# Optimization experiments

Hardware: AMD Instinct MI355X
Metric: run time of the kernel (lower is better)

The kernel has to match this reference:

```python
import jax, jax.numpy as jnp
import numpy as np

VOCAB = 32000
D = 512        # input_dim == hid_dim
HID = 512
LAYERS = 2
B = 64
S = 2048
PAD = 0


def setup_inputs() -> dict:
    key = jax.random.key(0)
    ks = jax.random.split(key, 6)
    # indices in [1, VOCAB) so the padding row is never hit (PAD=0)
    src = jax.random.randint(ks[0], (B, S), 1, VOCAB, dtype=jnp.int64 if jax.config.read('jax_enable_x64') else jnp.int32)
    scale = 1.0 / np.sqrt(HID)
    embed = jax.random.normal(ks[1], (VOCAB, D), dtype=jnp.float32)
    embed = embed.at[PAD].set(0.0)  # padding_idx row is zero
    # nn.RNN weights: per layer W_ih [HID, in], W_hh [HID, HID], b_ih, b_hh [HID]
    W_ih = jax.random.uniform(ks[2], (LAYERS, HID, D), jnp.float32, -scale, scale)
    W_hh = jax.random.uniform(ks[3], (LAYERS, HID, HID), jnp.float32, -scale, scale)
    b_ih = jax.random.uniform(ks[4], (LAYERS, HID), jnp.float32, -scale, scale)
    b_hh = jax.random.uniform(ks[5], (LAYERS, HID), jnp.float32, -scale, scale)
    return {"src": src, "embed": embed, "W_ih": W_ih, "W_hh": W_hh,
            "b_ih": b_ih, "b_hh": b_hh}


def reference(src, embed, W_ih, W_hh, b_ih, b_hh):
    # src: [B, S] -> transpose to time-major [S, B], then embedding lookup
    x = embed[src.T]                      # [S, B, D]
    finals = []
    for l in range(LAYERS):
        wi, wh = W_ih[l], W_hh[l]
        bi, bh = b_ih[l], b_hh[l]
        xb = jnp.einsum('sbd,hd->sbh', x, wi) + bi + bh  # precompute input term
        def step(h, x_t):
            h_new = jnp.tanh(x_t + h @ wh.T)
            return h_new, h_new
        h0 = jnp.zeros((x.shape[1], HID), dtype=x.dtype)
        hT, ys = jax.lax.scan(step, h0, xb)
        finals.append(hT)
        x = ys                             # feed layer output to next layer
    # nn.RNN returns hidden of shape [n_layers, batch, hid_dim]
    return jnp.stack(finals, axis=0)
```

## Files before the change

kernel.cpp:

```cpp
#include <hip/hip_runtime.h>


#define SEQ 2048

typedef _Float16 half8 __attribute__((ext_vector_type(8)));
typedef float floatx4 __attribute__((ext_vector_type(4)));
typedef unsigned long long u64;

__device__ inline half8 cvt8(const float* p) {
    float4 f0 = ((const float4*)p)[0];
    float4 f1 = ((const float4*)p)[1];
    half8 h;
    h[0]=(_Float16)f0.x; h[1]=(_Float16)f0.y; h[2]=(_Float16)f0.z; h[3]=(_Float16)f0.w;
    h[4]=(_Float16)f1.x; h[5]=(_Float16)f1.y; h[6]=(_Float16)f1.z; h[7]=(_Float16)f1.w;
    return h;
}

__device__ inline u64 ld8(const void* p) {
    return __hip_atomic_load((const u64*)p, __ATOMIC_RELAXED, __HIP_MEMORY_SCOPE_AGENT);
}
__device__ inline half8 ldfrag(const _Float16* p) {
    union { u64 d[2]; half8 h; } u;
    u.d[0] = ld8(p);
    u.d[1] = ld8(p + 4);
    return u.h;
}

#define MFMA(a, b, c) __builtin_amdgcn_mfma_f32_16x16x32_f16((a), (b), (c), 0, 0, 0)

__global__ __launch_bounds__(256, 1)
void rnn_persist(const int* __restrict__ src, const float* __restrict__ embed,
                 const float* __restrict__ W_ih, const float* __restrict__ W_hh,
                 const float* __restrict__ b_ih, const float* __restrict__ b_hh,
                 float* __restrict__ out, _Float16* hbase, int* flags)
{
    const int tid = threadIdx.x;
    if (tid >= 64) return;

    const int lane = tid;
    const int g    = blockIdx.x;
    const int L    = g >> 7;
    const int bg   = (g >> 5) & 3;
    const int jg   = g & 31;
    const int q    = lane >> 4;
    const int rr   = lane & 15;
    const int col  = jg * 16 + rr;

    _Float16* h0s = hbase;
    _Float16* h1s = hbase + 4 * 64 * 512;

    half8 bw[32];
    {
        const float* Wi = W_ih + ((size_t)L * 512 + col) * 512;
        const float* Wh = W_hh + ((size_t)L * 512 + col) * 512;
        #pragma unroll
        for (int u = 0; u < 16; ++u) bw[u]      = cvt8(Wi + u * 32 + q * 8);
        #pragma unroll
        for (int u = 0; u < 16; ++u) bw[16 + u] = cvt8(Wh + u * 32 + q * 8);
    }
    const float bias = b_ih[L * 512 + col] + b_hh[L * 512 + col];

    const int arow = bg * 16 + rr;
    int* flg = flags + bg * 64;
    const int lf = lane >> 5;

    for (int t = 0; t < SEQ; ++t) {
        floatx4 acc0 = {0.f,0.f,0.f,0.f}, acc1 = {0.f,0.f,0.f,0.f};

        if (L == 0) {
            const int erow = src[arow * SEQ + t];
            const float* eb = embed + (size_t)erow * 512 + q * 8;
            half8 ax[16];
            #pragma unroll
            for (int u = 0; u < 16; ++u) ax[u] = cvt8(eb + u * 32);
            #pragma unroll
            for (int u = 0; u < 16; ++u) {
                if (u & 1) acc1 = MFMA(ax[u], bw[u], acc1);
                else       acc0 = MFMA(ax[u], bw[u], acc0);
            }
            const int tgt = (lf == 0) ? t : (t - 3);
            for (long it = 0; it < (1L << 26); ++it) {
                int v = __hip_atomic_load(&flg[lane], __ATOMIC_RELAXED,
                                          __HIP_MEMORY_SCOPE_AGENT);
                if (__ballot(v >= tgt) == ~0ull) break;
                __builtin_amdgcn_s_sleep(1);
            }
            __atomic_signal_fence(__ATOMIC_SEQ_CST);
            if (t > 0) {
                const _Float16* hb = h0s + ((t - 1) & 3) * (64 * 512)
                                   + arow * 512 + q * 8;
                half8 ah[16];
                #pragma unroll
                for (int u = 0; u < 16; ++u) ah[u] = ldfrag(hb + u * 32);
                #pragma unroll
                for (int u = 0; u < 16; ++u) {
                    if (u & 1) acc1 = MFMA(ah[u], bw[16 + u], acc1);
                    else       acc0 = MFMA(ah[u], bw[16 + u], acc0);
                }
            }
        } else {
            const int tgt = (lf == 0) ? (t + 1) : t;
            for (long it = 0; it < (1L << 26); ++it) {
                int v = __hip_atomic_load(&flg[lane], __ATOMIC_RELAXED,
                                          __HIP_MEMORY_SCOPE_AGENT);
                if (__ballot(v >= tgt) == ~0ull) break;
                __builtin_amdgcn_s_sleep(1);
            }
            __atomic_signal_fence(__ATOMIC_SEQ_CST);
            {
                const _Float16* xa = h0s + (t & 3) * (64 * 512)
                                   + arow * 512 + q * 8;
                half8 ax[16];
                #pragma unroll
                for (int u = 0; u < 16; ++u) ax[u] = ldfrag(xa + u * 32);
                #pragma unroll
                for (int u = 0; u < 16; ++u) {
                    if (u & 1) acc1 = MFMA(ax[u], bw[u], acc1);
                    else       acc0 = MFMA(ax[u], bw[u], acc0);
                }
            }
            if (t > 0) {
                const _Float16* hb = h1s + ((t - 1) & 3) * (64 * 512)
                                   + arow * 512 + q * 8;
                half8 ah[16];
                #pragma unroll
                for (int u = 0; u < 16; ++u) ah[u] = ldfrag(hb + u * 32);
                #pragma unroll
                for (int u = 0; u < 16; ++u) {
                    if (u & 1) acc1 = MFMA(ah[u], bw[16 + u], acc1);
                    else       acc0 = MFMA(ah[u], bw[16 + u], acc0);
                }
            }
        }

        float hv[4];
        #pragma unroll
        for (int r = 0; r < 4; ++r)
            hv[r] = tanhf(acc0[r] + acc1[r] + bias);

        if (t == SEQ - 1) {
            #pragma unroll
            for (int r = 0; r < 4; ++r)
                out[(size_t)L * 64 * 512 + (size_t)(bg * 16 + q * 4 + r) * 512 + col]
                    = hv[r];
        }

        {
            _Float16* hw = ((L == 0) ? h0s : h1s) + (t & 3) * (64 * 512)
                         + (size_t)(bg * 16) * 512 + col;
            #pragma unroll
            for (int r = 0; r < 4; ++r) {
                union { _Float16 f; unsigned short u; } cv;
                cv.f = (_Float16)hv[r];
                __hip_atomic_store((unsigned short*)(hw + (q * 4 + r) * 512),
                                   cv.u, __ATOMIC_RELAXED,
                                   __HIP_MEMORY_SCOPE_AGENT);
            }
        }
        __atomic_signal_fence(__ATOMIC_SEQ_CST);
        __builtin_amdgcn_s_waitcnt(0);
        __atomic_signal_fence(__ATOMIC_SEQ_CST);
        if (lane == 0)
            __hip_atomic_store(&flg[L * 32 + jg], t + 1, __ATOMIC_RELAXED,
                               __HIP_MEMORY_SCOPE_AGENT);
    }
}

extern "C" void kernel_launch(void* const* d_in, const int* in_sizes, int n_in,
                              void* d_out, int out_size, void* d_ws, size_t ws_size,
                              hipStream_t stream) {
    const int*   src   = (const int*)  d_in[0];
    const float* embed = (const float*)d_in[1];
    const float* W_ih  = (const float*)d_in[2];
    const float* W_hh  = (const float*)d_in[3];
    const float* b_ih  = (const float*)d_in[4];
    const float* b_hh  = (const float*)d_in[5];
    float*     out   = (float*)d_out;
    int*       flags = (int*)d_ws;
    _Float16*  hbase = (_Float16*)((char*)d_ws + 16384);

    hipMemsetAsync(d_ws, 0, 16384, stream);

    rnn_persist<<<dim3(256), dim3(256), 0, stream>>>(
        src, embed, W_ih, W_hh, b_ih, b_hh, out, hbase, flags);
}
```

Before: 15.58 ms.

## Place each batch group's RNN tiles on one XCD with plain volatile sync

Each block reads its XCD id, and a grid-wide barrier lets every block see the full block-to-XCD map. The four XCDs holding the most blocks each take one batch group, and four waves per block each run a tile, so all producer/consumer flag and hidden-state traffic for a batch group stays inside one XCD's L2. Within an XCD the flags and hidden states use plain volatile loads and stores instead of agent-scope atomics. The next step's embedding load is also moved after the flag store so it overlaps the wait. The change relies on same-XCD L2 coherence for volatile accesses and adds a startup barrier. If the map is unsuitable it falls back to the atomic path, and both paths gain a spin timeout that can silently abort.

```diff
diff --git a/kernel.cpp b/kernel.cpp
--- a/kernel.cpp
+++ b/kernel.cpp
@@ -6,6 +6,8 @@
 typedef _Float16 half8 __attribute__((ext_vector_type(8)));
 typedef float floatx4 __attribute__((ext_vector_type(4)));
 typedef unsigned long long u64;
+
+#define MFMA(a, b, c) __builtin_amdgcn_mfma_f32_16x16x32_f16((a), (b), (c), 0, 0, 0)
 
 __device__ inline half8 cvt8(const float* p) {
     float4 f0 = ((const float4*)p)[0];
@@ -16,38 +18,53 @@
     return h;
 }
 
-__device__ inline u64 ld8(const void* p) {
-    return __hip_atomic_load((const u64*)p, __ATOMIC_RELAXED, __HIP_MEMORY_SCOPE_AGENT);
-}
-__device__ inline half8 ldfrag(const _Float16* p) {
-    union { u64 d[2]; half8 h; } u;
-    u.d[0] = ld8(p);
-    u.d[1] = ld8(p + 4);
-    return u.h;
-}
-
-#define MFMA(a, b, c) __builtin_amdgcn_mfma_f32_16x16x32_f16((a), (b), (c), 0, 0, 0)
-
-__global__ __launch_bounds__(256, 1)
-void rnn_persist(const int* __restrict__ src, const float* __restrict__ embed,
-                 const float* __restrict__ W_ih, const float* __restrict__ W_hh,
-                 const float* __restrict__ b_ih, const float* __restrict__ b_hh,
-                 float* __restrict__ out, _Float16* hbase, int* flags)
+__device__ inline int xcc_id(void) {
+    int x;
+    asm volatile("s_getreg_b32 %0, hwreg(HW_REG_XCC_ID)" : "=s"(x));
+    return x & 7;
+}
+
+__device__ inline int f_ldflag(const int* p) { return *(volatile const int*)p; }
+__device__ inline void f_stflag(int* p, int v) { *(volatile int*)p = v; }
+__device__ inline void f_sth2(_Float16* p, _Float16 v) { *(volatile _Float16*)p = v; }
+__device__ inline void f_ldfrag(const _Float16* p, half8 a[16]) {
+    #pragma unroll
+    for (int u = 0; u < 16; ++u) a[u] = *(volatile const half8*)(p + u * 32);
+}
+
+__device__ inline int a_ldflag(const int* p) {
+    return __hip_atomic_load(p, __ATOMIC_RELAXED, __HIP_MEMORY_SCOPE_AGENT);
+}
+__device__ inline void a_stflag(int* p, int v) {
+    __hip_atomic_store(p, v, __ATOMIC_RELAXED, __HIP_MEMORY_SCOPE_AGENT);
+}
+__device__ inline void a_sth2(_Float16* p, _Float16 v) {
+    union { _Float16 f; unsigned short s; } c; c.f = v;
+    __hip_atomic_store((unsigned short*)p, c.s, __ATOMIC_RELAXED,
+                       __HIP_MEMORY_SCOPE_AGENT);
+}
+__device__ inline void a_ldfrag(const _Float16* p, half8 a[16]) {
+    #pragma unroll
+    for (int u = 0; u < 16; ++u) {
+        union { u64 d[2]; half8 h; } x;
+        x.d[0] = __hip_atomic_load((const u64*)(p + u * 32),
+                                   __ATOMIC_RELAXED, __HIP_MEMORY_SCOPE_AGENT);
+        x.d[1] = __hip_atomic_load((const u64*)(p + u * 32) + 1,
+                                   __ATOMIC_RELAXED, __HIP_MEMORY_SCOPE_AGENT);
+        a[u] = x.h;
+    }
+}
+
+template <bool FAST>
+__device__ void run_rnn(int L, int jg, int bg, int lane,
+                        const int* __restrict__ src, const float* __restrict__ embed,
+                        const float* __restrict__ W_ih, const float* __restrict__ W_hh,
+                        const float* __restrict__ b_ih, const float* __restrict__ b_hh,
+                        float* __restrict__ out, _Float16* hbase, int* flags)
 {
-    const int tid = threadIdx.x;
-    if (tid >= 64) return;
-
-    const int lane = tid;
-    const int g    = blockIdx.x;
-    const int L    = g >> 7;
-    const int bg   = (g >> 5) & 3;
-    const int jg   = g & 31;
-    const int q    = lane >> 4;
-    const int rr   = lane & 15;
-    const int col  = jg * 16 + rr;
-
-    _Float16* h0s = hbase;
-    _Float16* h1s = hbase + 4 * 64 * 512;
+    const int q   = lane >> 4;
+    const int rr  = lane & 15;
+    const int col = jg * 16 + rr;
 
     half8 bw[32];
     {
@@ -60,38 +77,42 @@
     }
     const float bias = b_ih[L * 512 + col] + b_hh[L * 512 + col];
 
-    const int arow = bg * 16 + rr;
-    int* flg = flags + bg * 64;
-    const int lf = lane >> 5;
-
-    for (int t = 0; t < SEQ; ++t) {
+    _Float16* hbg = hbase + (size_t)bg * 65536;
+    int* flg   = flags + bg * 1024;
+    int* stamp = flg + L * 32 + jg;
+
+    half8 ax[16];
+    if (L == 0) {
+        const int erow = src[(bg * 16 + rr) * SEQ + 0];
+        const float* eb = embed + (size_t)erow * 512 + q * 8;
+        #pragma unroll
+        for (int u = 0; u < 16; ++u) ax[u] = cvt8(eb + u * 32);
+    }
+
+    bool dead = false;
+    for (int t = 0; t < SEQ && !dead; ++t) {
         floatx4 acc0 = {0.f,0.f,0.f,0.f}, acc1 = {0.f,0.f,0.f,0.f};
 
         if (L == 0) {
-            const int erow = src[arow * SEQ + t];
-            const float* eb = embed + (size_t)erow * 512 + q * 8;
-            half8 ax[16];
-            #pragma unroll
-            for (int u = 0; u < 16; ++u) ax[u] = cvt8(eb + u * 32);
             #pragma unroll
             for (int u = 0; u < 16; ++u) {
                 if (u & 1) acc1 = MFMA(ax[u], bw[u], acc1);
                 else       acc0 = MFMA(ax[u], bw[u], acc0);
             }
-            const int tgt = (lf == 0) ? t : (t - 3);
-            for (long it = 0; it < (1L << 26); ++it) {
-                int v = __hip_atomic_load(&flg[lane], __ATOMIC_RELAXED,
-                                          __HIP_MEMORY_SCOPE_AGENT);
+            const int tgt = (lane < 32) ? t : (t - 3);
+            int it = 0;
+            while (true) {
+                int v = FAST ? f_ldflag(flg + lane) : a_ldflag(flg + lane);
                 if (__ballot(v >= tgt) == ~0ull) break;
+                if (++it > (1 << 22)) { dead = true; break; }
                 __builtin_amdgcn_s_sleep(1);
             }
+            if (dead) break;
             __atomic_signal_fence(__ATOMIC_SEQ_CST);
             if (t > 0) {
-                const _Float16* hb = h0s + ((t - 1) & 3) * (64 * 512)
-                                   + arow * 512 + q * 8;
+                const _Float16* hp = hbg + ((t - 1) & 3) * 8192 + rr * 512 + q * 8;
                 half8 ah[16];
-                #pragma unroll
-                for (int u = 0; u < 16; ++u) ah[u] = ldfrag(hb + u * 32);
+                if (FAST) f_ldfrag(hp, ah); else a_ldfrag(hp, ah);
                 #pragma unroll
                 for (int u = 0; u < 16; ++u) {
                     if (u & 1) acc1 = MFMA(ah[u], bw[16 + u], acc1);
@@ -99,32 +120,31 @@
                 }
             }
         } else {
-            const int tgt = (lf == 0) ? (t + 1) : t;
-            for (long it = 0; it < (1L << 26); ++it) {
-                int v = __hip_atomic_load(&flg[lane], __ATOMIC_RELAXED,
-                                          __HIP_MEMORY_SCOPE_AGENT);
+            const int tgt = (lane < 32) ? (t + 1) : t;
+            int it = 0;
+            while (true) {
+                int v = FAST ? f_ldflag(flg + lane) : a_ldflag(flg + lane);
                 if (__ballot(v >= tgt) == ~0ull) break;
+                if (++it > (1 << 22)) { dead = true; break; }
                 __builtin_amdgcn_s_sleep(1);
             }
+            if (dead) break;
             __atomic_signal_fence(__ATOMIC_SEQ_CST);
             {
-                const _Float16* xa = h0s + (t & 3) * (64 * 512)
-                                   + arow * 512 + q * 8;
-                half8 ax[16];
-                #pragma unroll
-                for (int u = 0; u < 16; ++u) ax[u] = ldfrag(xa + u * 32);
+                const _Float16* xp = hbg + (t & 3) * 8192 + rr * 512 + q * 8;
+                half8 xa[16];
+                if (FAST) f_ldfrag(xp, xa); else a_ldfrag(xp, xa);
                 #pragma unroll
                 for (int u = 0; u < 16; ++u) {
-                    if (u & 1) acc1 = MFMA(ax[u], bw[u], acc1);
-                    else       acc0 = MFMA(ax[u], bw[u], acc0);
+                    if (u & 1) acc1 = MFMA(xa[u], bw[u], acc1);
+                    else       acc0 = MFMA(xa[u], bw[u], acc0);
                 }
             }
             if (t > 0) {
-                const _Float16* hb = h1s + ((t - 1) & 3) * (64 * 512)
-                                   + arow * 512 + q * 8;
+                const _Float16* hp = hbg + 32768 + ((t - 1) & 3) * 8192
+                                   + rr * 512 + q * 8;
                 half8 ah[16];
-                #pragma unroll
-                for (int u = 0; u < 16; ++u) ah[u] = ldfrag(hb + u * 32);
+                if (FAST) f_ldfrag(hp, ah); else a_ldfrag(hp, ah);
                 #pragma unroll
                 for (int u = 0; u < 16; ++u) {
                     if (u & 1) acc1 = MFMA(ah[u], bw[16 + u], acc1);
@@ -146,23 +166,100 @@
         }
 
         {
-            _Float16* hw = ((L == 0) ? h0s : h1s) + (t & 3) * (64 * 512)
-                         + (size_t)(bg * 16) * 512 + col;
+            _Float16* hw = hbg + (L ? 32768 : 0) + (t & 3) * 8192 + col;
             #pragma unroll
             for (int r = 0; r < 4; ++r) {
-                union { _Float16 f; unsigned short u; } cv;
-                cv.f = (_Float16)hv[r];
-                __hip_atomic_store((unsigned short*)(hw + (q * 4 + r) * 512),
-                                   cv.u, __ATOMIC_RELAXED,
-                                   __HIP_MEMORY_SCOPE_AGENT);
+                if (FAST) f_sth2(hw + (q * 4 + r) * 512, (_Float16)hv[r]);
+                else      a_sth2(hw + (q * 4 + r) * 512, (_Float16)hv[r]);
             }
         }
         __atomic_signal_fence(__ATOMIC_SEQ_CST);
         __builtin_amdgcn_s_waitcnt(0);
         __atomic_signal_fence(__ATOMIC_SEQ_CST);
-        if (lane == 0)
-            __hip_atomic_store(&flg[L * 32 + jg], t + 1, __ATOMIC_RELAXED,
+        if (lane == 0) {
+            if (FAST) f_stflag(stamp, t + 1); else a_stflag(stamp, t + 1);
+        }
+
+        if (L == 0 && t + 1 < SEQ) {
+            const int erow = src[(bg * 16 + rr) * SEQ + (t + 1)];
+            const float* eb = embed + (size_t)erow * 512 + q * 8;
+            #pragma unroll
+            for (int u = 0; u < 16; ++u) ax[u] = cvt8(eb + u * 32);
+        }
+    }
+}
+
+__global__ __launch_bounds__(256, 1)
+void rnn_v9(const int* __restrict__ src, const float* __restrict__ embed,
+            const float* __restrict__ W_ih, const float* __restrict__ W_hh,
+            const float* __restrict__ b_ih, const float* __restrict__ b_hh,
+            float* __restrict__ out, _Float16* hbase, int* flags,
+            int* xcdmap, int* barcnt)
+{
+    __shared__ int smap[256];
+    __shared__ int s_top[4];
+    __shared__ int s_ok;
+
+    const int tid = threadIdx.x;
+    const int bid = blockIdx.x;
+    const int xcd = xcc_id();
+
+    if (tid == 0) {
+        __hip_atomic_store(&xcdmap[bid], xcd + 1, __ATOMIC_RELAXED,
+                           __HIP_MEMORY_SCOPE_AGENT);
+        __builtin_amdgcn_s_waitcnt(0);
+        __hip_atomic_fetch_add(barcnt, 1, __ATOMIC_RELAXED,
                                __HIP_MEMORY_SCOPE_AGENT);
+        int it = 0;
+        while (__hip_atomic_load(barcnt, __ATOMIC_RELAXED,
+                                 __HIP_MEMORY_SCOPE_AGENT) < 256) {
+            if (++it > (1 << 22)) break;
+            __builtin_amdgcn_s_sleep(2);
+        }
+    }
+    __syncthreads();
+
+    smap[tid] = __hip_atomic_load(&xcdmap[tid], __ATOMIC_RELAXED,
+                                  __HIP_MEMORY_SCOPE_AGENT) - 1;
+    __syncthreads();
+    if (tid == 0) {
+        int cnt[8] = {0,0,0,0,0,0,0,0};
+        bool bad = false;
+        for (int i = 0; i < 256; ++i) {
+            int x = smap[i];
+            if (x < 0 || x > 7) { bad = true; break; }
+            cnt[x]++;
+        }
+        int order[8] = {0,1,2,3,4,5,6,7};
+        for (int a = 0; a < 4 && !bad; ++a) {
+            int best = a;
+            for (int b = a + 1; b < 8; ++b)
+                if (cnt[order[b]] > cnt[order[best]]) best = b;
+            int tmp = order[a]; order[a] = order[best]; order[best] = tmp;
+            if (cnt[order[a]] < 16) bad = true;
+            s_top[a] = order[a];
+        }
+        s_ok = bad ? 0 : 1;
+    }
+    __syncthreads();
+
+    const bool fast = (s_ok == 1);
+    if (fast) {
+        int slotIdx = -1;
+        #pragma unroll
+        for (int a = 0; a < 4; ++a) if (s_top[a] == xcd) slotIdx = a;
+        if (slotIdx < 0) return;
+        int rank = 0;
+        for (int i = 0; i < bid; ++i) if (smap[i] == xcd) rank++;
+        if (rank >= 16) return;
+        const int w    = tid >> 6;
+        const int tile = rank * 4 + w;
+        run_rnn<true>(tile >> 5, tile & 31, slotIdx, tid & 63,
+                      src, embed, W_ih, W_hh, b_ih, b_hh, out, hbase, flags);
+    } else {
+        if (tid >= 64) return;
+        run_rnn<false>(bid >> 7, bid & 31, (bid >> 5) & 3, tid,
+                       src, embed, W_ih, W_hh, b_ih, b_hh, out, hbase, flags);
     }
 }
 
@@ -175,12 +272,14 @@
     const float* W_hh  = (const float*)d_in[3];
     const float* b_ih  = (const float*)d_in[4];
     const float* b_hh  = (const float*)d_in[5];
-    float*     out   = (float*)d_out;
-    int*       flags = (int*)d_ws;
-    _Float16*  hbase = (_Float16*)((char*)d_ws + 16384);
-
-    hipMemsetAsync(d_ws, 0, 16384, stream);
-
-    rnn_persist<<<dim3(256), dim3(256), 0, stream>>>(
-        src, embed, W_ih, W_hh, b_ih, b_hh, out, hbase, flags);
-}
+    float*     out    = (float*)d_out;
+    int*       barcnt = (int*)d_ws;
+    int*       xcdmap = (int*)d_ws + 64;
+    int*       flags  = (int*)((char*)d_ws + 4096);
+    _Float16*  hbase  = (_Float16*)((char*)d_ws + 65536);
+
+    hipMemsetAsync(d_ws, 0, 20480, stream);
+
+    rnn_v9<<<dim3(256), dim3(256), 0, stream>>>(
+        src, embed, W_ih, W_hh, b_ih, b_hh, out, hbase, flags, xcdmap, barcnt);
+}
```

Result: slower. 24.15 ms (+55.0%).
